# Performance work log

Measured on AMD Instinct MI355X. Metric: run time of the kernel, lower is better.

The kernel has to match this reference:

```python
import math
import jax, jax.numpy as jnp
import numpy as np

IN_CH = 256
BIG, SMALL = 15, 3
GHOST_RATIO = 0.23
NK = math.ceil(BIG / SMALL)           # 5
PAD = SMALL // 2                       # 1
MID = BIG // 2                         # 7
REAL_PAD = [MID - i * SMALL - PAD for i in range(NK)]  # [6,3,0,-3,-6]

# Replicate the torch module's deterministic ghost/rep channel split
np.random.seed(123)
_ghostN = int(IN_CH * GHOST_RATIO)     # 58
REPN = IN_CH - _ghostN                 # 198
_ghost = np.sort(np.random.choice(IN_CH, _ghostN, replace=False))
_rep = np.array(sorted(set(range(IN_CH)) - set(_ghost.tolist())), dtype=np.int64)

B, L = 32, 4096
EPS = 1e-5


def _bn(x, g, b):
    # training-mode BatchNorm1d over (B, L) per channel
    m = jnp.mean(x, (0, 2), keepdims=True)
    v = jnp.var(x, (0, 2), keepdims=True)
    return (x - m) * jax.lax.rsqrt(v + EPS) * g[None, :, None] + b[None, :, None]


def _shift(x, p):
    # zero-filled shift along L: out[t] = x[t - p]
    Lx = x.shape[-1]
    if p > 0:
        return jnp.pad(x, ((0, 0), (0, 0), (p, 0)))[..., :Lx]
    if p < 0:
        return jnp.pad(x, ((0, 0), (0, 0), (0, -p)))[..., -Lx:]
    return x


def setup_inputs() -> dict:
    key = jax.random.key(0)
    ks = jax.random.split(key, 3)
    inputs = jax.random.normal(ks[0], (B, IN_CH, L), dtype=jnp.float32)
    lora_w1 = jax.random.normal(ks[1], (REPN * NK, 1, SMALL), dtype=jnp.float32) * 0.1
    lora_w2 = jax.random.normal(ks[2], (REPN * NK, 1, SMALL), dtype=jnp.float32) * 0.1
    ones = jnp.ones((REPN,), jnp.float32)
    zeros = jnp.zeros((REPN,), jnp.float32)
    return {"inputs": inputs, "lora_w1": lora_w1, "lora_w2": lora_w2,
            "gamma1": ones, "beta1": zeros, "gamma2": ones, "beta2": zeros,
            "gamma3": ones, "beta3": zeros}


def reference(inputs, lora_w1, lora_w2, gamma1, beta1, gamma2, beta2, gamma3, beta3):
    rep_in = inputs[:, _rep, :]        # [B, repN, L]
    ghost_in = inputs[:, _ghost, :]    # [B, ghostN, L]
    # sum of N_path depthwise convs == one conv with summed weights
    w = lora_w1 + lora_w2              # [repN*nk, 1, small]
    out = jax.lax.conv_general_dilated(
        rep_in, w, window_strides=(1,), padding=[(PAD, PAD)],
        dimension_numbers=("NCH", "OIH", "NCH"), feature_group_count=REPN)
    b, _, l = out.shape
    o = out.reshape(b, REPN, NK, l)    # torch grouped conv: group-major channel order
    # shift-add decomposition: reconstruct big-kernel responses from nk small-conv slices
    x1 = sum(_shift(o[:, :, i, :], REAL_PAD[i]) for i in range(NK))
    x2 = sum(_shift(o[:, :, i, :], -REAL_PAD[i]) for i in range(NK))
    x3 = o[:, :, NK // 2, :]           # zero-shift (small-kernel) slice
    x1 = _bn(x1, gamma1, beta1)
    x2 = _bn(x2, gamma2, beta2)
    x3 = _bn(x3, gamma3, beta3)
    x = x1 + x2 + x3 + rep_in
    return jnp.concatenate([x, ghost_in], axis=1)  # [B, C, L]
```

## Files before the change

### kernel.cpp

```cpp
#include <hip/hip_runtime.h>
#include <hip/hip_bf16.h>

#define LEN 4096
#define BATCH 32
#define CH 256
#define REPN 198
#define GHOSTN 58
#define NROW (REPN * BATCH)
#define NGHOST (GHOSTN * BATCH)
#define P1REPBLK 1584

typedef float f32x4 __attribute__((ext_vector_type(4)));

struct MTState { unsigned mt[624]; int mti; };
struct Tab { int rep[REPN]; int ghost[GHOSTN]; };

static constexpr unsigned mt_next(MTState& s) {
    if (s.mti >= 624) {
        for (int k = 0; k < 624; ++k) {
            unsigned y = (s.mt[k] & 0x80000000u) | (s.mt[(k + 1) % 624] & 0x7fffffffu);
            s.mt[k] = s.mt[(k + 397) % 624] ^ (y >> 1) ^ ((y & 1u) ? 0x9908b0dfu : 0u);
        }
        s.mti = 0;
    }
    unsigned y = s.mt[s.mti++];
    y ^= y >> 11;
    y ^= (y << 7) & 0x9d2c5680u;
    y ^= (y << 15) & 0xefc60000u;
    y ^= y >> 18;
    return y;
}

static constexpr Tab make_tab() {
    MTState s{};
    s.mt[0] = 123u;
    for (int i = 1; i < 624; ++i)
        s.mt[i] = 1812433253u * (s.mt[i - 1] ^ (s.mt[i - 1] >> 30)) + (unsigned)i;
    s.mti = 624;
    int perm[256] = {};
    for (int i = 0; i < 256; ++i) perm[i] = i;
    for (int i = 255; i > 0; --i) {
        unsigned mask = (unsigned)i;
        mask |= mask >> 1; mask |= mask >> 2; mask |= mask >> 4;
        mask |= mask >> 8; mask |= mask >> 16;
        unsigned j = 0;
        do { j = mt_next(s) & mask; } while (j > (unsigned)i);
        int t = perm[i]; perm[i] = perm[j]; perm[j] = t;
    }
    bool g[256] = {};
    for (int k = 0; k < GHOSTN; ++k) g[perm[k]] = true;
    Tab t{};
    int rc = 0, gc = 0;
    for (int c = 0; c < 256; ++c) {
        if (g[c]) t.ghost[gc++] = c;
        else      t.rep[rc++] = c;
    }
    return t;
}

__constant__ Tab d_tab = make_tab();

__device__ __forceinline__ void load_fast(const float* __restrict__ row, int e, float* v) {
    const f32x4* q4 = (const f32x4*)(row + e - 8);
#pragma unroll
    for (int t = 0; t < 5; ++t) {
        f32x4 u = q4[t];
        v[4 * t] = u.x; v[4 * t + 1] = u.y; v[4 * t + 2] = u.z; v[4 * t + 3] = u.w;
    }
}

__device__ __forceinline__ void load_slow(const float* __restrict__ row, int e, float* v) {
#pragma unroll
    for (int d = 0; d < 20; ++d) {
        int fi = e - 8 + d;
        v[d] = ((unsigned)fi < (unsigned)LEN) ? row[fi] : 0.f;
    }
}

__global__ __launch_bounds__(256) void pass1_kernel(const float* __restrict__ x,
                                                    const float* __restrict__ w1,
                                                    const float* __restrict__ w2,
                                                    float* __restrict__ stats_ws,
                                                    float* __restrict__ out) {
    const int blk = blockIdx.x;
    if (blk >= P1REPBLK) {
        const int g = (blk - P1REPBLK) % GHOSTN;
        const int b = (blk - P1REPBLK) / GHOSTN;
        const int ch = d_tab.ghost[g];
        const f32x4* src = (const f32x4*)(x + ((size_t)b * CH + ch) * LEN);
        f32x4* dst = (f32x4*)(out + ((size_t)b * CH + REPN + g) * LEN);
#pragma unroll
        for (int k = 0; k < 4; ++k) {
            f32x4 t = __builtin_nontemporal_load(&src[threadIdx.x + 256 * k]);
            dst[threadIdx.x + 256 * k] = t;
        }
        return;
    }

    const int wv = (blk << 2) | (threadIdx.x >> 6);
    const int lane = threadIdx.x & 63;
    const int r = wv % REPN;
    const int b = wv / REPN;
    const float* row = x + ((size_t)b * CH + d_tab.rep[r]) * LEN;

    float wb[5][3];
    {
        const float* p1 = w1 + r * 15;
        const float* p2 = w2 + r * 15;
#pragma unroll
        for (int i = 0; i < 5; ++i)
#pragma unroll
            for (int t = 0; t < 3; ++t) wb[i][t] = p1[i * 3 + t] + p2[i * 3 + t];
    }

    float s1 = 0, s1q = 0, s2 = 0, s2q = 0, s3 = 0, s3q = 0;
    float v[20];

#define STATQ(E, GATED)                                                           \
    {                                                                             \
        _Pragma("unroll")                                                         \
        for (int j = 0; j < 4; ++j) {                                             \
            const int l = (E) + j;                                                \
            float x1 = 0.f, x2 = 0.f, x3 = 0.f;                                   \
            _Pragma("unroll")                                                     \
            for (int i = 0; i < 5; ++i) {                                         \
                float a1 = fmaf(wb[i][0], v[j + 1 + 3 * i],                       \
                           fmaf(wb[i][1], v[j + 2 + 3 * i],                       \
                                wb[i][2] * v[j + 3 + 3 * i]));                    \
                float a2 = fmaf(wb[i][0], v[j + 13 - 3 * i],                      \
                           fmaf(wb[i][1], v[j + 14 - 3 * i],                      \
                                wb[i][2] * v[j + 15 - 3 * i]));                   \
                if (i == 2) x3 = a1;                                 \
                if (GATED) {                                                      \
                    a1 = ((unsigned)(l - 6 + 3 * i) < (unsigned)LEN) ? a1 : 0.f;  \
                    a2 = ((unsigned)(l + 6 - 3 * i) < (unsigned)LEN) ? a2 : 0.f;  \
                }                                                                 \
                x1 += a1; x2 += a2;                                               \
            }                                                                     \
            s1 += x1; s1q = fmaf(x1, x1, s1q);                                    \
            s2 += x2; s2q = fmaf(x2, x2, s2q);                                    \
            s3 += x3; s3q = fmaf(x3, x3, s3q);                                    \
        }                                                                         \
    }

    {
        const int e = 4 * lane;
        if (lane < 2) { load_slow(row, e, v); STATQ(e, true); }
        else          { load_fast(row, e, v); STATQ(e, false); }
    }
#pragma unroll 2
    for (int k = 1; k < 15; ++k) {
        const int e = 4 * lane + 256 * k;
        load_fast(row, e, v);
        STATQ(e, false);
    }
    {
        const int e = 4 * lane + 3840;
        if (lane >= 62) { load_slow(row, e, v); STATQ(e, true); }
        else            { load_fast(row, e, v); STATQ(e, false); }
    }
#undef STATQ

#pragma unroll
    for (int off = 32; off > 0; off >>= 1) {
        s1 += __shfl_down(s1, off);  s1q += __shfl_down(s1q, off);
        s2 += __shfl_down(s2, off);  s2q += __shfl_down(s2q, off);
        s3 += __shfl_down(s3, off);  s3q += __shfl_down(s3q, off);
    }
    if (lane == 0) {
        stats_ws[(0 * REPN + r) * BATCH + b] = s1;
        stats_ws[(1 * REPN + r) * BATCH + b] = s1q;
        stats_ws[(2 * REPN + r) * BATCH + b] = s2;
        stats_ws[(3 * REPN + r) * BATCH + b] = s2q;
        stats_ws[(4 * REPN + r) * BATCH + b] = s3;
        stats_ws[(5 * REPN + r) * BATCH + b] = s3q;
    }
}

__global__ __launch_bounds__(256) void pass2_kernel(const float* __restrict__ x,
                                                    const float* __restrict__ w1,
                                                    const float* __restrict__ w2,
                                                    const float* __restrict__ stats_ws,
                                                    const float* __restrict__ g1, const float* __restrict__ b1,
                                                    const float* __restrict__ g2, const float* __restrict__ b2,
                                                    const float* __restrict__ g3, const float* __restrict__ b3,
                                                    float* __restrict__ out) {
    const int wv = (blockIdx.x << 2) | (threadIdx.x >> 6);
    const int lane = threadIdx.x & 63;
    const int r = wv % REPN;
    const int b = wv / REPN;
    const int ch = d_tab.rep[r];
    const float* row = x + ((size_t)b * CH + ch) * LEN;

    float p[6];
    const int bb = lane & 31;
#pragma unroll
    for (int q = 0; q < 6; ++q) p[q] = stats_ws[(q * REPN + r) * BATCH + bb];
#pragma unroll
    for (int m = 1; m < 32; m <<= 1)
#pragma unroll
        for (int q = 0; q < 6; ++q) p[q] += __shfl_xor(p[q], m);

    const double invN = 1.0 / (double)(BATCH * LEN);
    float sc[3], sh[3];
    {
        const float gr[3] = {g1[r], g2[r], g3[r]};
        const float br[3] = {b1[r], b2[r], b3[r]};
#pragma unroll
        for (int q = 0; q < 3; ++q) {
            double mean = (double)p[2 * q] * invN;
            double var = (double)p[2 * q + 1] * invN - mean * mean;
            double inv = 1.0 / sqrt(var + 1e-5);
            double scale = (double)gr[q] * inv;
            sc[q] = (float)scale;
            sh[q] = (float)((double)br[q] - mean * scale);
        }
    }
    const float base = sh[0] + sh[1] + sh[2];

    float wb[5][3];
    const float* p1 = w1 + r * 15;
    const float* p2 = w2 + r * 15;
#pragma unroll
    for (int i = 0; i < 5; ++i)
#pragma unroll
        for (int t = 0; t < 3; ++t) wb[i][t] = p1[i * 3 + t] + p2[i * 3 + t];

    float c[15];
#pragma unroll
    for (int k = 0; k < 5; ++k)
#pragma unroll
        for (int t = 0; t < 3; ++t)
            c[3 * k + t] = fmaf(sc[0], wb[k][t], sc[1] * wb[4 - k][t]);
#pragma unroll
    for (int t = 0; t < 3; ++t) c[6 + t] = fmaf(sc[2], wb[2][t], c[6 + t]);

    float* orow = out + ((size_t)b * CH + r) * LEN;
    float v[20];

#define INTERIOR_QUAD(E)                                                          \
    {                                                                             \
        float o[4];                                                               \
        _Pragma("unroll")                                                         \
        for (int j = 0; j < 4; ++j) {                                             \
            float acc = base + v[j + 8];                                          \
            _Pragma("unroll")                                                     \
            for (int d = 0; d < 15; ++d) acc = fmaf(c[d], v[j + 1 + d], acc);     \
            o[j] = acc;                                                           \
        }                                                                         \
        f32x4 t = {o[0], o[1], o[2], o[3]};                                       \
        *(f32x4*)(orow + (E)) = t;                                                \
    }

#define EDGE_QUAD(E)                                                              \
    {                                                                             \
        float o[4];                                                               \
        _Pragma("unroll")                                                         \
        for (int j = 0; j < 4; ++j) {                                             \
            const int l = (E) + j;                                                \
            float x1 = 0.f, x2 = 0.f, x3 = 0.f;                                   \
            _Pragma("unroll")                                                     \
            for (int i = 0; i < 5; ++i) {                                         \
                float a1 = fmaf(wb[i][0], v[j + 1 + 3 * i],                       \
                           fmaf(wb[i][1], v[j + 2 + 3 * i],                       \
                                wb[i][2] * v[j + 3 + 3 * i]));                    \
                float a2 = fmaf(wb[i][0], v[j + 13 - 3 * i],                      \
                           fmaf(wb[i][1], v[j + 14 - 3 * i],                      \
                                wb[i][2] * v[j + 15 - 3 * i]));                   \
                if (i == 2) x3 = a1;                                              \
                a1 = ((unsigned)(l - 6 + 3 * i) < (unsigned)LEN) ? a1 : 0.f;      \
                a2 = ((unsigned)(l + 6 - 3 * i) < (unsigned)LEN) ? a2 : 0.f;      \
                x1 += a1; x2 += a2;                                               \
            }                                                                     \
            o[j] = fmaf(sc[0], x1, fmaf(sc[1], x2, fmaf(sc[2], x3, base + v[j + 8]))); \
        }                                                                         \
        f32x4 t = {o[0], o[1], o[2], o[3]};                                       \
        *(f32x4*)(orow + (E)) = t;                                                \
    }

    {
        const int e = 4 * lane;
        if (lane < 2) { load_slow(row, e, v); EDGE_QUAD(e); }
        else          { load_fast(row, e, v); INTERIOR_QUAD(e); }
    }
#pragma unroll
    for (int k = 1; k < 15; ++k) {
        const int e = 4 * lane + 256 * k;
        load_fast(row, e, v);
        INTERIOR_QUAD(e);
    }
    {
        const int e = 4 * lane + 3840;
        if (lane >= 62) { load_slow(row, e, v); EDGE_QUAD(e); }
        else            { load_fast(row, e, v); INTERIOR_QUAD(e); }
    }
#undef INTERIOR_QUAD
#undef EDGE_QUAD
}

extern "C" void kernel_launch(void* const* d_in, const int* in_sizes, int n_in,
                              void* d_out, int out_size, void* d_ws, size_t ws_size,
                              hipStream_t stream) {
    const float* x  = (const float*)d_in[0];
    const float* w1 = (const float*)d_in[1];
    const float* w2 = (const float*)d_in[2];
    const float* g1 = (const float*)d_in[3];
    const float* b1 = (const float*)d_in[4];
    const float* g2 = (const float*)d_in[5];
    const float* b2 = (const float*)d_in[6];
    const float* g3 = (const float*)d_in[7];
    const float* b3 = (const float*)d_in[8];
    float* out = (float*)d_out;
    float* stats_ws = (float*)d_ws;

    pass1_kernel<<<P1REPBLK + NGHOST, 256, 0, stream>>>(x, w1, w2, stats_ws, out);
    pass2_kernel<<<1584, 256, 0, stream>>>(x, w1, w2, stats_ws,
                                           g1, b1, g2, b2, g3, b3, out);
}
```

Measured before the change: 91.36 us.

## Compute BN statistics via input autocorrelation instead of explicit convolution outputs

Pass 1 no longer evaluates the shifted convolution sums per position to accumulate sum and sum-of-squares. It accumulates the input row sum and 15 lagged autocorrelation terms per lane, then derives each branch's sum and sum of squares from products of weight correlations with these lags. A separate correction path on 26 lanes handles the boundary positions where zero-padding gates break the identity. This trades per-element FMA work for 15 extra register accumulators and a larger shuffle reduction, and changes floating-point summation order.

```diff
diff --git a/kernel.cpp b/kernel.cpp
--- a/kernel.cpp
+++ b/kernel.cpp
@@ -1,5 +1,4 @@
 #include <hip/hip_runtime.h>
-#include <hip/hip_bf16.h>
 
 #define LEN 4096
 #define BATCH 32
@@ -60,22 +59,8 @@
 
 __constant__ Tab d_tab = make_tab();
 
-__device__ __forceinline__ void load_fast(const float* __restrict__ row, int e, float* v) {
-    const f32x4* q4 = (const f32x4*)(row + e - 8);
-#pragma unroll
-    for (int t = 0; t < 5; ++t) {
-        f32x4 u = q4[t];
-        v[4 * t] = u.x; v[4 * t + 1] = u.y; v[4 * t + 2] = u.z; v[4 * t + 3] = u.w;
-    }
-}
-
-__device__ __forceinline__ void load_slow(const float* __restrict__ row, int e, float* v) {
-#pragma unroll
-    for (int d = 0; d < 20; ++d) {
-        int fi = e - 8 + d;
-        v[d] = ((unsigned)fi < (unsigned)LEN) ? row[fi] : 0.f;
-    }
-}
+#define C1F(D) wb[(D) / 3][(D) % 3]
+#define C2F(D) wb[4 - (D) / 3][(D) % 3]
 
 __global__ __launch_bounds__(256) void pass1_kernel(const float* __restrict__ x,
                                                     const float* __restrict__ w1,
@@ -103,6 +88,55 @@
     const int b = wv / REPN;
     const float* row = x + ((size_t)b * CH + d_tab.rep[r]) * LEN;
 
+    float A[15];
+#pragma unroll
+    for (int dl = 0; dl < 15; ++dl) A[dl] = 0.f;
+    float SX = 0.f;
+    float B0[16], B1[16];
+    const int base = lane << 6;
+
+#define LOADV16(DST, OFF)                                                         \
+    {                                                                             \
+        if ((OFF) < LEN) {                                                        \
+            const f32x4* q4_ = (const f32x4*)(row + (OFF));                       \
+            _Pragma("unroll")                                                     \
+            for (int t = 0; t < 4; ++t) {                                         \
+                f32x4 u_ = q4_[t];                                                \
+                DST[4 * t] = u_.x; DST[4 * t + 1] = u_.y;                         \
+                DST[4 * t + 2] = u_.z; DST[4 * t + 3] = u_.w;                     \
+            }                                                                     \
+        } else {                                                                  \
+            _Pragma("unroll")                                                     \
+            for (int t = 0; t < 16; ++t) DST[t] = 0.f;                            \
+        }                                                                         \
+    }
+
+#define ACC16(LO, HI)                                                             \
+    {                                                                             \
+        _Pragma("unroll")                                                         \
+        for (int j = 0; j < 16; ++j) {                                            \
+            const float xj_ = LO[j];                                              \
+            SX += xj_;                                                            \
+            _Pragma("unroll")                                                     \
+            for (int dl = 0; dl < 15; ++dl) {                                     \
+                const float xd_ = (j + dl < 16) ? LO[j + dl] : HI[j + dl - 16];   \
+                A[dl] = fmaf(xj_, xd_, A[dl]);                                    \
+            }                                                                     \
+        }                                                                         \
+    }
+
+    LOADV16(B0, base);
+    LOADV16(B1, base + 16);
+    ACC16(B0, B1);
+    LOADV16(B0, base + 32);
+    ACC16(B1, B0);
+    LOADV16(B1, base + 48);
+    ACC16(B0, B1);
+    LOADV16(B0, base + 64);
+    ACC16(B1, B0);
+#undef LOADV16
+#undef ACC16
+
     float wb[5][3];
     {
         const float* p1 = w1 + r * 15;
@@ -113,67 +147,90 @@
             for (int t = 0; t < 3; ++t) wb[i][t] = p1[i * 3 + t] + p2[i * 3 + t];
     }
 
-    float s1 = 0, s1q = 0, s2 = 0, s2q = 0, s3 = 0, s3q = 0;
-    float v[20];
-
-#define STATQ(E, GATED)                                                           \
-    {                                                                             \
-        _Pragma("unroll")                                                         \
-        for (int j = 0; j < 4; ++j) {                                             \
-            const int l = (E) + j;                                                \
-            float x1 = 0.f, x2 = 0.f, x3 = 0.f;                                   \
-            _Pragma("unroll")                                                     \
-            for (int i = 0; i < 5; ++i) {                                         \
-                float a1 = fmaf(wb[i][0], v[j + 1 + 3 * i],                       \
-                           fmaf(wb[i][1], v[j + 2 + 3 * i],                       \
-                                wb[i][2] * v[j + 3 + 3 * i]));                    \
-                float a2 = fmaf(wb[i][0], v[j + 13 - 3 * i],                      \
-                           fmaf(wb[i][1], v[j + 14 - 3 * i],                      \
-                                wb[i][2] * v[j + 15 - 3 * i]));                   \
-                if (i == 2) x3 = a1;                                 \
-                if (GATED) {                                                      \
-                    a1 = ((unsigned)(l - 6 + 3 * i) < (unsigned)LEN) ? a1 : 0.f;  \
-                    a2 = ((unsigned)(l + 6 - 3 * i) < (unsigned)LEN) ? a2 : 0.f;  \
-                }                                                                 \
-                x1 += a1; x2 += a2;                                               \
-            }                                                                     \
-            s1 += x1; s1q = fmaf(x1, x1, s1q);                                    \
-            s2 += x2; s2q = fmaf(x2, x2, s2q);                                    \
-            s3 += x3; s3q = fmaf(x3, x3, s3q);                                    \
-        }                                                                         \
-    }
-
-    {
-        const int e = 4 * lane;
-        if (lane < 2) { load_slow(row, e, v); STATQ(e, true); }
-        else          { load_fast(row, e, v); STATQ(e, false); }
-    }
-#pragma unroll 2
-    for (int k = 1; k < 15; ++k) {
-        const int e = 4 * lane + 256 * k;
-        load_fast(row, e, v);
-        STATQ(e, false);
-    }
-    {
-        const int e = 4 * lane + 3840;
-        if (lane >= 62) { load_slow(row, e, v); STATQ(e, true); }
-        else            { load_fast(row, e, v); STATQ(e, false); }
-    }
-#undef STATQ
+    float d1 = 0.f, d1q = 0.f, d2 = 0.f, d2q = 0.f, d3 = 0.f, d3q = 0.f;
+    if (lane < 26) {
+        const int l = (lane <= 12) ? (lane - 7) : (4090 + (lane - 13));
+        float u1 = 0.f, u2 = 0.f, u3 = 0.f, g1 = 0.f, g2 = 0.f;
+#pragma unroll
+        for (int d = 0; d < 15; ++d) {
+            const int p = l + d - 7;
+            const float xd = ((unsigned)p < (unsigned)LEN) ? row[p] : 0.f;
+            const float a1 = C1F(d) * xd;
+            const float a2 = C2F(d) * xd;
+            u1 += a1; u2 += a2;
+            if (d >= 6 && d <= 8) u3 += a1;
+            const bool gate = ((unsigned)(l - 6 + 3 * (d / 3)) < (unsigned)LEN);
+            g1 += gate ? a1 : 0.f;
+            g2 += gate ? a2 : 0.f;
+        }
+        if ((unsigned)l < (unsigned)LEN) {
+            d1 = g1 - u1;  d1q = fmaf(g1, g1, -u1 * u1);
+            d2 = g2 - u2;  d2q = fmaf(g2, g2, -u2 * u2);
+        } else {
+            d1 = -u1;  d1q = -u1 * u1;
+            d2 = -u2;  d2q = -u2 * u2;
+            d3 = -u3;  d3q = -u3 * u3;
+        }
+    }
 
 #pragma unroll
     for (int off = 32; off > 0; off >>= 1) {
-        s1 += __shfl_down(s1, off);  s1q += __shfl_down(s1q, off);
-        s2 += __shfl_down(s2, off);  s2q += __shfl_down(s2q, off);
-        s3 += __shfl_down(s3, off);  s3q += __shfl_down(s3q, off);
-    }
+#pragma unroll
+        for (int dl = 0; dl < 15; ++dl) A[dl] += __shfl_down(A[dl], off);
+        SX += __shfl_down(SX, off);
+        d1 += __shfl_down(d1, off);   d1q += __shfl_down(d1q, off);
+        d2 += __shfl_down(d2, off);   d2q += __shfl_down(d2q, off);
+        d3 += __shfl_down(d3, off);   d3q += __shfl_down(d3q, off);
+    }
+
     if (lane == 0) {
-        stats_ws[(0 * REPN + r) * BATCH + b] = s1;
-        stats_ws[(1 * REPN + r) * BATCH + b] = s1q;
-        stats_ws[(2 * REPN + r) * BATCH + b] = s2;
-        stats_ws[(3 * REPN + r) * BATCH + b] = s2q;
-        stats_ws[(4 * REPN + r) * BATCH + b] = s3;
-        stats_ws[(5 * REPN + r) * BATCH + b] = s3q;
+        float sq1 = 0.f, sq2 = 0.f;
+#pragma unroll
+        for (int dl = 0; dl < 15; ++dl) {
+            float r1 = 0.f, r2 = 0.f;
+#pragma unroll
+            for (int d = 0; d + dl < 15; ++d) {
+                r1 = fmaf(C1F(d), C1F(d + dl), r1);
+                r2 = fmaf(C2F(d), C2F(d + dl), r2);
+            }
+            const float wA = (dl ? 2.f : 1.f) * A[dl];
+            sq1 = fmaf(r1, wA, sq1);
+            sq2 = fmaf(r2, wA, sq2);
+        }
+        const float c30 = wb[2][0], c31 = wb[2][1], c32 = wb[2][2];
+        float sq3 = (c30 * c30 + c31 * c31 + c32 * c32) * A[0]
+                  + 2.f * (c30 * c31 + c31 * c32) * A[1]
+                  + 2.f * (c30 * c32) * A[2];
+        float cs = 0.f;
+#pragma unroll
+        for (int i = 0; i < 5; ++i)
+#pragma unroll
+            for (int t = 0; t < 3; ++t) cs += wb[i][t];
+        const float c3s = c30 + c31 + c32;
+
+        stats_ws[(0 * REPN + r) * BATCH + b] = fmaf(cs, SX, d1);
+        stats_ws[(1 * REPN + r) * BATCH + b] = sq1 + d1q;
+        stats_ws[(2 * REPN + r) * BATCH + b] = fmaf(cs, SX, d2);
+        stats_ws[(3 * REPN + r) * BATCH + b] = sq2 + d2q;
+        stats_ws[(4 * REPN + r) * BATCH + b] = fmaf(c3s, SX, d3);
+        stats_ws[(5 * REPN + r) * BATCH + b] = sq3 + d3q;
+    }
+}
+
+__device__ __forceinline__ void load_fast(const float* __restrict__ row, int e, float* v) {
+    const f32x4* q4 = (const f32x4*)(row + e - 8);
+#pragma unroll
+    for (int t = 0; t < 5; ++t) {
+        f32x4 u = q4[t];
+        v[4 * t] = u.x; v[4 * t + 1] = u.y; v[4 * t + 2] = u.z; v[4 * t + 3] = u.w;
+    }
+}
+
+__device__ __forceinline__ void load_slow(const float* __restrict__ row, int e, float* v) {
+#pragma unroll
+    for (int d = 0; d < 20; ++d) {
+        int fi = e - 8 + d;
+        v[d] = ((unsigned)fi < (unsigned)LEN) ? row[fi] : 0.f;
     }
 }
 
```

Measured after the change: 85.98 us. 1.06x faster.
